# Optimization experiments

Hardware: AMD Instinct MI355X
Metric: run time of the kernel (lower is better)

The kernel has to match this reference:

```python
import jax, jax.numpy as jnp
import numpy as np

S, B, D, H = 2048, 2, 1024, 16
E = D // H  # per-head hidden dim = 64
MASK_VAL = 1e18


def setup_inputs() -> dict:
    rng = jax.random.key(0)
    ks = jax.random.split(rng, 12)
    query = jax.random.normal(ks[0], (S, B, D), dtype=jnp.float32)
    key = jax.random.normal(ks[1], (S, B, D), dtype=jnp.float32)
    value = jax.random.normal(ks[2], (S, B, D), dtype=jnp.float32)
    key_mask = jax.random.randint(ks[3], (S, B), 0, 2).astype(bool)
    # per-head Linear weights stacked: torch Linear is y = x @ W.T + b, W: [out, in]
    Wq = jax.random.normal(ks[4], (H, E, D), dtype=jnp.float32) * 0.02
    bq = jax.random.normal(ks[5], (H, E), dtype=jnp.float32) * 0.02
    Wk = jax.random.normal(ks[6], (H, E, D), dtype=jnp.float32) * 0.02
    bk = jax.random.normal(ks[7], (H, E), dtype=jnp.float32) * 0.02
    Wv = jax.random.normal(ks[8], (H, E, D), dtype=jnp.float32) * 0.02
    bv = jax.random.normal(ks[9], (H, E), dtype=jnp.float32) * 0.02
    Wo = jax.random.normal(ks[10], (D, D), dtype=jnp.float32) * 0.02
    bo = jax.random.normal(ks[11], (D,), dtype=jnp.float32) * 0.02
    return {"query": query, "key": key, "value": value, "key_mask": key_mask,
            "Wq": Wq, "bq": bq, "Wk": Wk, "bk": bk, "Wv": Wv, "bv": bv,
            "Wo": Wo, "bo": bo}


def reference(query, key, value, key_mask, Wq, bq, Wk, bk, Wv, bv, Wo, bo):
    # per-head projections, batched over heads: [S, B, H, E]
    q = jnp.einsum('imd,hed->imhe', query, Wq) + bq
    k = jnp.einsum('imd,hed->imhe', key, Wk) + bk
    v = jnp.einsum('imd,hed->imhe', value, Wv) + bv
    # scores: [H, S_q, B, S_k], scaled by sqrt(per-head dim)
    scores = jnp.einsum('imhe,jmhe->himj', q, k) / jnp.sqrt(jnp.float32(E))
    # key padding mask: key_mask [j, m] -> transpose to [m, j], broadcast over h, i
    scores = scores - key_mask.astype(jnp.float32).T * MASK_VAL
    # causal (forward) mask: strict upper triangle [i, j]
    fwd_mask = jnp.triu(jnp.ones((S, S), dtype=jnp.float32), k=1) * MASK_VAL
    scores = scores - fwd_mask[None, :, None, :]
    attn = jax.nn.softmax(scores, axis=-1)
    # weighted sum: [S, B, H, E]; reshape concatenates heads in order (h outer)
    out = jnp.einsum('himj,jmhe->imhe', attn, v).reshape(S, B, H * E)
    return out @ Wo.T + bo
```

## Files before the change

kernel.cpp:

```cpp
#include <hip/hip_runtime.h>
#include <cmath>

namespace {

constexpr int S = 2048, B = 2, D = 1024, H = 16, E = 64;
constexpr int RM = S * B;
constexpr int K = D;
constexpr int KVB = 64;
constexpr int SEGS_PER_HM = 48;

constexpr float QSCL = 0.18033688011112043f;
constexpr float KMB2 = 1.4426950408889634e18f;

using s16x8 = __attribute__((ext_vector_type(8))) short;
using u16x8 = __attribute__((ext_vector_type(8))) unsigned short;
using f32x4 = __attribute__((ext_vector_type(4))) float;
using u32x2 = __attribute__((ext_vector_type(2))) unsigned;
typedef unsigned short ushort;
typedef unsigned int u32;

__constant__ unsigned char SEG_ORDER[48] = {
    17,0,1,16,44,46,47,15,40,42,43,45,14,36,38,39,41,13,32,34,35,37,
    12,28,30,31,33,11,24,26,27,29,10,20,22,23,25,9,18,19,21,8,7,6,5,4,3,2};

__device__ inline f32x4 mfma16(s16x8 a, s16x8 b, f32x4 c) {
    return __builtin_amdgcn_mfma_f32_16x16x32_bf16(a, b, c, 0, 0, 0);
}

__device__ inline ushort f2bf(float f) {
    unsigned u = __builtin_bit_cast(unsigned, f);
    u += 0x7fffu + ((u >> 16) & 1u);
    return (ushort)(u >> 16);
}

__device__ inline u32 cvtpk_bf16(float lo, float hi) {
    u32 r;
    asm("v_cvt_pk_bf16_f32 %0, %1, %2" : "=v"(r) : "v"(lo), "v"(hi));
    return r;
}

__device__ inline float fexp2(float x) {
#if __has_builtin(__builtin_amdgcn_exp2f)
    return __builtin_amdgcn_exp2f(x);
#else
    return exp2f(x);
#endif
}

__device__ inline void gload_lds16(const void* g, void* l) {
    __builtin_amdgcn_global_load_lds(
        (const __attribute__((address_space(1))) u32*)g,
        (__attribute__((address_space(3))) u32*)l,
        16, 0, 0);
}

__global__ __launch_bounds__(256)
void cvt3_kernel(const float* __restrict__ a, const float* __restrict__ b,
                 const float* __restrict__ c,
                 ushort* __restrict__ ao, ushort* __restrict__ bo2, ushort* __restrict__ co)
{
    const float* src = (blockIdx.y == 0) ? a : (blockIdx.y == 1) ? b : c;
    ushort* dst      = (blockIdx.y == 0) ? ao : (blockIdx.y == 1) ? bo2 : co;
    const size_t i = ((size_t)blockIdx.x * 256 + threadIdx.x) * 8;
    float4 x = *reinterpret_cast<const float4*>(&src[i]);
    float4 y = *reinterpret_cast<const float4*>(&src[i + 4]);
    u16x8 o;
    o[0]=f2bf(x.x); o[1]=f2bf(x.y); o[2]=f2bf(x.z); o[3]=f2bf(x.w);
    o[4]=f2bf(y.x); o[5]=f2bf(y.y); o[6]=f2bf(y.z); o[7]=f2bf(y.w);
    *reinterpret_cast<u16x8*>(&dst[i]) = o;
}

__global__ __launch_bounds__(256)
void cvt4_kernel(const float* __restrict__ a, const float* __restrict__ b,
                 const float* __restrict__ c, const float* __restrict__ d,
                 ushort* __restrict__ ao, ushort* __restrict__ bo2,
                 ushort* __restrict__ co, ushort* __restrict__ dd)
{
    const float* src = (blockIdx.y == 0) ? a : (blockIdx.y == 1) ? b : (blockIdx.y == 2) ? c : d;
    ushort* dst      = (blockIdx.y == 0) ? ao : (blockIdx.y == 1) ? bo2 : (blockIdx.y == 2) ? co : dd;
    const size_t i = ((size_t)blockIdx.x * 256 + threadIdx.x) * 8;
    float4 x = *reinterpret_cast<const float4*>(&src[i]);
    float4 y = *reinterpret_cast<const float4*>(&src[i + 4]);
    u16x8 o;
    o[0]=f2bf(x.x); o[1]=f2bf(x.y); o[2]=f2bf(x.z); o[3]=f2bf(x.w);
    o[4]=f2bf(y.x); o[5]=f2bf(y.y); o[6]=f2bf(y.z); o[7]=f2bf(y.w);
    *reinterpret_cast<u16x8*>(&dst[i]) = o;
}

__device__ inline void mm_core2(const ushort* __restrict__ A, const ushort* __restrict__ W,
                                ushort* Albuf, ushort* Blbuf, int r0, int n0,
                                f32x4 (&acc)[4][2])
{
    const int t  = threadIdx.x;
    const int w  = t >> 6, l = t & 63;
    const int lr = l & 15, lg = l >> 4;
    const int wr = w >> 2, wc = w & 3;
    const int srow = t >> 3;
    const int gch  = (t & 7) ^ (srow & 7);

    auto STAGE = [&](int buf, int kt) {
        #pragma unroll
        for (int c = 0; c < 2; ++c) {
            gload_lds16(&A[(size_t)(r0 + c * 64 + srow) * K + kt + gch * 8],
                        (char*)Albuf + buf * 16384 + c * 8192 + t * 16);
            gload_lds16(&W[(size_t)(n0 + c * 64 + srow) * K + kt + gch * 8],
                        (char*)Blbuf + buf * 16384 + c * 8192 + t * 16);
        }
    };

    STAGE(0, 0);
    __syncthreads();
    int cur = 0;

    for (int kt = 0; kt < K; kt += 64) {
        if (kt + 64 < K) STAGE(cur ^ 1, kt + 64);
        const char* Ab = (const char*)Albuf + cur * 16384;
        const char* Bb = (const char*)Blbuf + cur * 16384;

        #pragma unroll
        for (int ks = 0; ks < 2; ++ks) {
            s16x8 af[4], bf[2];
            #pragma unroll
            for (int mf = 0; mf < 4; ++mf) {
                const int row = wr * 64 + mf * 16 + lr;
                const int ch  = (ks * 4 + lg) ^ (row & 7);
                af[mf] = *reinterpret_cast<const s16x8*>(Ab + row * 128 + ch * 16);
            }
            #pragma unroll
            for (int nf = 0; nf < 2; ++nf) {
                const int row = wc * 32 + nf * 16 + lr;
                const int ch  = (ks * 4 + lg) ^ (row & 7);
                bf[nf] = *reinterpret_cast<const s16x8*>(Bb + row * 128 + ch * 16);
            }
            #pragma unroll
            for (int mf = 0; mf < 4; ++mf)
                #pragma unroll
                for (int nf = 0; nf < 2; ++nf)
                    acc[mf][nf] = mfma16(af[mf], bf[nf], acc[mf][nf]);
        }
        __syncthreads();
        cur ^= 1;
    }
}

__global__ __launch_bounds__(512)
void proj_gemm(const ushort* __restrict__ qa, const ushort* __restrict__ ka,
               const ushort* __restrict__ va,
               const ushort* __restrict__ wq, const ushort* __restrict__ wk,
               const ushort* __restrict__ wv,
               const float* __restrict__ bq, const float* __restrict__ bk,
               const float* __restrict__ bv,
               ushort* __restrict__ qd, ushort* __restrict__ kd, ushort* __restrict__ vtd)
{
    __shared__ ushort Albuf[2 * 128 * 64];
    __shared__ ushort Blbuf[2 * 128 * 64];
    const int z = blockIdx.z;
    const ushort* A    = (z == 0) ? qa : (z == 1) ? ka : va;
    const ushort* W    = (z == 0) ? wq : (z == 1) ? wk : wv;
    const float*  bias = (z == 0) ? bq : (z == 1) ? bk : bv;
    const int r0 = blockIdx.x * 128, n0 = blockIdx.y * 128;

    f32x4 acc[4][2] = {};
    mm_core2(A, W, Albuf, Blbuf, r0, n0, acc);

    const int t = threadIdx.x, w = t >> 6, l = t & 63, lr = l & 15, lg = l >> 4;
    const int wr = w >> 2, wc = w & 3;
    #pragma unroll
    for (int mf = 0; mf < 4; ++mf) {
        #pragma unroll
        for (int nf = 0; nf < 2; ++nf) {
            const int n = n0 + wc * 32 + nf * 16 + lr;
            const int h = n >> 6, e = n & 63;
            const float bb = bias[n];
            #pragma unroll
            for (int rg = 0; rg < 4; ++rg) {
                const int r = r0 + wr * 64 + mf * 16 + lg * 4 + rg;
                const int i = r >> 1, m = r & 1;
                const ushort val = f2bf(acc[mf][nf][rg] + bb);
                if (z < 2) {
                    ushort* dst = (z == 0) ? qd : kd;
                    dst[(((size_t)(h * B + m)) * S + i) * E + e] = val;
                } else {
                    vtd[(((size_t)(h * B + m)) * E + e) * S + i] = val;
                }
            }
        }
    }
}

__global__ __launch_bounds__(512)
void out_gemm(const ushort* __restrict__ A, const ushort* __restrict__ W,
              const float* __restrict__ bias, float* __restrict__ Cout)
{
    __shared__ ushort Albuf[2 * 128 * 64];
    __shared__ ushort Blbuf[2 * 128 * 64];
    const int r0 = blockIdx.x * 128, n0 = blockIdx.y * 128;

    f32x4 acc[4][2] = {};
    mm_core2(A, W, Albuf, Blbuf, r0, n0, acc);

    const int t = threadIdx.x, w = t >> 6, l = t & 63, lr = l & 15, lg = l >> 4;
    const int wr = w >> 2, wc = w & 3;
    #pragma unroll
    for (int mf = 0; mf < 4; ++mf) {
        #pragma unroll
        for (int nf = 0; nf < 2; ++nf) {
            const int n = n0 + wc * 32 + nf * 16 + lr;
            const float bb = bias[n];
            #pragma unroll
            for (int rg = 0; rg < 4; ++rg) {
                const int r = r0 + wr * 64 + mf * 16 + lg * 4 + rg;
                Cout[(size_t)r * D + n] = acc[mf][nf][rg] + bb;
            }
        }
    }
}

__global__ __launch_bounds__(256)
void prescan_kernel(const int* __restrict__ km, int* __restrict__ fu,
                    float* __restrict__ kmf)
{
    __shared__ int red[256];
    const int m = blockIdx.x, t = threadIdx.x;
    int best = S;
    for (int j = t; j < S; j += 256) {
        const int v = km[(size_t)j * B + m];
        kmf[(size_t)m * S + j] = v ? KMB2 : 0.0f;
        if (v == 0) best = min(best, j);
    }
    red[t] = best;
    __syncthreads();
    for (int s = 128; s > 0; s >>= 1) {
        if (t < s) red[t] = min(red[t], red[t + s]);
        __syncthreads();
    }
    if (t == 0) fu[m] = red[0];
}

__device__ inline int nseg_of(int t)  { return (t == 0 || t >= 17) ? 2 : 1; }
__device__ inline int segoff_of(int t){ return (t == 0) ? 0 : (t <= 16 ? t + 1 : 2 * t - 16); }

__global__ __launch_bounds__(256)
void attn_seg(const ushort* __restrict__ q, const ushort* __restrict__ k,
              const ushort* __restrict__ vt, const int* __restrict__ fu,
              const float* __restrict__ kmf,
              float* __restrict__ part_O, float* __restrict__ part_ml)
{
    const int s = SEG_ORDER[blockIdx.x];
    const int m = blockIdx.y, h = blockIdx.z;
    int t, kk;
    if (s < 2)       { t = 0;               kk = s; }
    else if (s < 18) { t = s - 1;           kk = 0; }
    else             { t = 17 + ((s - 18) >> 1); kk = (s - 18) & 1; }
    const int i0 = t * 64;
    const int hm = h * B + m;
    const int seg = hm * SEGS_PER_HM + s;

    const int ns = nseg_of(t);
    const int h1 = (t == 0) ? 16 : ((t + 2) >> 1);
    const int jendT = (fu[m] <= i0) ? (t + 1) : 32;
    const int lo = (ns == 2 && kk == 1) ? h1 : 0;
    const int hi = (ns == 2 && kk == 0) ? min(h1, jendT) : jendT;

    const ushort* Qb  = q  + (size_t)hm * S * E;
    const ushort* Kb  = k  + (size_t)hm * S * E;
    const ushort* Vtb = vt + (size_t)hm * E * S;
    const float*  kmfm = kmf + (size_t)m * S;

    __shared__ ushort Ks[2][KVB * 64];
    __shared__ ushort Vts[2][E * 64];
    __shared__ ushort Pw[4][16 * 64];

    const int tid = threadIdx.x;
    const int wv  = tid >> 6;
    const int l   = tid & 63;
    const int lg  = l >> 4;
    const int lcc = l & 15;
    const int a7  = lcc & 7;
    const int gi  = i0 + wv * 16 + lcc;

    const int srow = tid >> 3;
    const int sch  = (tid & 7) ^ (srow & 7);

    s16x8 qf0, qf1;
    {
        const ushort* qp = &Qb[(size_t)gi * E + lg * 8];
        qf0 = *reinterpret_cast<const s16x8*>(qp);
        qf1 = *reinterpret_cast<const s16x8*>(qp + 32);
    }

    float m_run = -INFINITY, l_run = 0.0f;
    f32x4 oacc[4] = {};

    auto STAGE = [&](int buf, int tj) {
        const int j0 = tj * 64;
        gload_lds16(&Kb[(size_t)(j0 + srow) * E + sch * 8],
                    (char*)&Ks[buf][0] + tid * 16);
        gload_lds16(&Kb[(size_t)(j0 + 32 + srow) * E + sch * 8],
                    (char*)&Ks[buf][0] + 4096 + tid * 16);
        gload_lds16(&Vtb[(size_t)srow * S + j0 + sch * 8],
                    (char*)&Vts[buf][0] + tid * 16);
        gload_lds16(&Vtb[(size_t)(32 + srow) * S + j0 + sch * 8],
                    (char*)&Vts[buf][0] + 4096 + tid * 16);
    };

    STAGE(0, lo);
    __syncthreads();
    int cur = 0;

    for (int tj = lo; tj < hi; ++tj) {
        const int j0 = tj * 64;
        if (tj + 1 < hi) STAGE(cur ^ 1, tj + 1);

        float4 km4[4];
        #pragma unroll
        for (int jt = 0; jt < 4; ++jt)
            km4[jt] = *reinterpret_cast<const float4*>(&kmfm[j0 + jt * 16 + lg * 4]);

        f32x4 sacc[4];
        #pragma unroll
        for (int jt = 0; jt < 4; ++jt) {
            const char* kb = (const char*)&Ks[cur][0] + (jt * 16 + lcc) * 128;
            s16x8 kf0 = *reinterpret_cast<const s16x8*>(kb + (lg ^ a7) * 16);
            s16x8 kf1 = *reinterpret_cast<const s16x8*>(kb + ((lg ^ a7) ^ 4) * 16);
            f32x4 a = {};
            a = mfma16(kf0, qf0, a);
            a = mfma16(kf1, qf1, a);
            sacc[jt] = a;
        }

        if (j0 >= i0) {
            #pragma unroll
            for (int jt = 0; jt < 4; ++jt) {
                const int jmi = j0 + jt * 16 + lg * 4 - gi;
                #pragma unroll
                for (int r = 0; r < 4; ++r) {
                    float sc = fmaf(sacc[jt][r], QSCL, -((const float*)&km4[jt])[r]);
                    sc -= (jmi + r > 0) ? KMB2 : 0.0f;
                    sacc[jt][r] = sc;
                }
            }
        } else {
            #pragma unroll
            for (int jt = 0; jt < 4; ++jt)
                #pragma unroll
                for (int r = 0; r < 4; ++r)
                    sacc[jt][r] = fmaf(sacc[jt][r], QSCL, -((const float*)&km4[jt])[r]);
        }

        float mm = -INFINITY;
        #pragma unroll
        for (int jt = 0; jt < 4; ++jt)
            #pragma unroll
            for (int r = 0; r < 4; ++r) mm = fmaxf(mm, sacc[jt][r]);
        mm = fmaxf(mm, __shfl_xor(mm, 16));
        mm = fmaxf(mm, __shfl_xor(mm, 32));

        if (!__all(mm <= m_run)) {
            const float m_new = fmaxf(m_run, mm);
            const float scale = fexp2(m_run - m_new);
            m_run = m_new;
            l_run *= scale;
            float scr[4];
            #pragma unroll
            for (int r = 0; r < 4; ++r)
                scr[r] = __shfl(scale, (l & 48) | (lg * 4 + r));
            #pragma unroll
            for (int et = 0; et < 4; ++et)
                #pragma unroll
                for (int r = 0; r < 4; ++r) oacc[et][r] *= scr[r];
        }

        float psum = 0.0f;
        #pragma unroll
        for (int jt = 0; jt < 4; ++jt) {
            const float p0 = fexp2(sacc[jt][0] - m_run);
            const float p1 = fexp2(sacc[jt][1] - m_run);
            const float p2 = fexp2(sacc[jt][2] - m_run);
            const float p3 = fexp2(sacc[jt][3] - m_run);
            psum += (p0 + p1) + (p2 + p3);
            const u32 w0 = cvtpk_bf16(p0, p1);
            const u32 w1 = cvtpk_bf16(p2, p3);
            const int pby = lcc * 128 + (((jt * 2 + (lg >> 1)) ^ a7) << 4) + ((lg & 1) << 3);
            *reinterpret_cast<u32x2*>((char*)&Pw[wv][0] + pby) = (u32x2){w0, w1};
        }
        psum += __shfl_xor(psum, 16);
        psum += __shfl_xor(psum, 32);
        l_run += psum;

        {
            const char* pb = (const char*)&Pw[wv][0] + lcc * 128;
            s16x8 pf0 = *reinterpret_cast<const s16x8*>(pb + (lg ^ a7) * 16);
            s16x8 pf1 = *reinterpret_cast<const s16x8*>(pb + ((lg ^ a7) ^ 4) * 16);
            #pragma unroll
            for (int et = 0; et < 4; ++et) {
                const char* vb = (const char*)&Vts[cur][0] + (et * 16 + lcc) * 128;
                s16x8 vf0 = *reinterpret_cast<const s16x8*>(vb + (lg ^ a7) * 16);
                s16x8 vf1 = *reinterpret_cast<const s16x8*>(vb + ((lg ^ a7) ^ 4) * 16);
                oacc[et] = mfma16(pf0, vf0, oacc[et]);
                oacc[et] = mfma16(pf1, vf1, oacc[et]);
            }
        }

        __syncthreads();
        cur ^= 1;
    }

    #pragma unroll
    for (int et = 0; et < 4; ++et)
        #pragma unroll
        for (int r = 0; r < 4; ++r)
            part_O[((size_t)seg * 64 + wv * 16 + lg * 4 + r) * 64 + et * 16 + lcc] = oacc[et][r];
    if (lg == 0) {
        part_ml[((size_t)seg * 64 + wv * 16 + lcc) * 2]     = m_run;
        part_ml[((size_t)seg * 64 + wv * 16 + lcc) * 2 + 1] = l_run;
    }
}

__global__ __launch_bounds__(256)
void attn_combine(const float* __restrict__ part_O, const float* __restrict__ part_ml,
                  ushort* __restrict__ a_ws)
{
    const int t = blockIdx.x, m = blockIdx.y, h = blockIdx.z;
    const int hm = h * B + m;
    const int ns = nseg_of(t);
    const int seg0 = hm * SEGS_PER_HM + segoff_of(t);

    const int tid = threadIdx.x;
    const int row = tid >> 2;
    const int e0  = (tid & 3) * 16;
    const int gi  = t * 64 + row;

    const size_t r0 = (size_t)seg0 * 64 + row;
    const float m0 = part_ml[r0 * 2], l0 = part_ml[r0 * 2 + 1];
    float w0, w1 = 0.0f, linv;
    size_t r1 = 0;
    if (ns == 2) {
        r1 = ((size_t)(seg0 + 1)) * 64 + row;
        const float m1 = part_ml[r1 * 2], l1 = part_ml[r1 * 2 + 1];
        const float ms = fmaxf(m0, m1);
        w0 = fexp2(m0 - ms);
        w1 = fexp2(m1 - ms);
        linv = 1.0f / (l0 * w0 + l1 * w1);
    } else {
        w0 = 1.0f;
        linv = 1.0f / l0;
    }

    ushort* dst = a_ws + ((size_t)gi * B + m) * D + h * E + e0;
    #pragma unroll
    for (int c = 0; c < 4; ++c) {
        float4 o0 = *reinterpret_cast<const float4*>(&part_O[r0 * 64 + e0 + c * 4]);
        float ov[4] = {o0.x, o0.y, o0.z, o0.w};
        if (ns == 2) {
            float4 o1 = *reinterpret_cast<const float4*>(&part_O[r1 * 64 + e0 + c * 4]);
            ov[0] = ov[0] * w0 + o1.x * w1;
            ov[1] = ov[1] * w0 + o1.y * w1;
            ov[2] = ov[2] * w0 + o1.z * w1;
            ov[3] = ov[3] * w0 + o1.w * w1;
        } else {
            ov[0] *= w0; ov[1] *= w0; ov[2] *= w0; ov[3] *= w0;
        }
        dst[c * 4 + 0] = f2bf(ov[0] * linv);
        dst[c * 4 + 1] = f2bf(ov[1] * linv);
        dst[c * 4 + 2] = f2bf(ov[2] * linv);
        dst[c * 4 + 3] = f2bf(ov[3] * linv);
    }
}

}

extern "C" void kernel_launch(void* const* d_in, const int* in_sizes, int n_in,
                              void* d_out, int out_size, void* d_ws, size_t ws_size,
                              hipStream_t stream)
{
    const float* query = (const float*)d_in[0];
    const float* key   = (const float*)d_in[1];
    const float* value = (const float*)d_in[2];
    const int*   kmask = (const int*)  d_in[3];
    const float* Wq    = (const float*)d_in[4];
    const float* bq    = (const float*)d_in[5];
    const float* Wk    = (const float*)d_in[6];
    const float* bk    = (const float*)d_in[7];
    const float* Wv    = (const float*)d_in[8];
    const float* bv    = (const float*)d_in[9];
    const float* Wo    = (const float*)d_in[10];
    const float* bo    = (const float*)d_in[11];
    float* out = (float*)d_out;

    const size_t act = (size_t)RM * D;
    const size_t wsz = (size_t)D * D;
    ushort* wob  = (ushort*)d_ws;
    ushort* wqb  = wob + wsz;
    ushort* wkb  = wqb + wsz;
    ushort* wvb  = wkb + wsz;
    ushort* qa   = wvb + wsz;
    ushort* ka   = qa + act;
    ushort* va   = ka + act;
    ushort* q_ws = va + act;
    ushort* k_ws = q_ws + act;
    ushort* vt_ws= k_ws + act;
    ushort* a_ws = vt_ws + act;
    float* part_O  = (float*)qa;
    float* part_ml = (float*)wqb;
    int*   fu      = (int*)wkb;
    float* kmf     = (float*)wkb + 8;

    cvt3_kernel<<<dim3(act / 8 / 256, 3), 256, 0, stream>>>(query, key, value, qa, ka, va);
    cvt4_kernel<<<dim3(wsz / 8 / 256, 4), 256, 0, stream>>>(Wq, Wk, Wv, Wo, wqb, wkb, wvb, wob);

    proj_gemm<<<dim3(RM / 128, D / 128, 3), 512, 0, stream>>>(
        qa, ka, va, wqb, wkb, wvb, bq, bk, bv, q_ws, k_ws, vt_ws);

    prescan_kernel<<<dim3(B), 256, 0, stream>>>(kmask, fu, kmf);

    attn_seg<<<dim3(SEGS_PER_HM, B, H), 256, 0, stream>>>(
        q_ws, k_ws, vt_ws, fu, kmf, part_O, part_ml);

    attn_combine<<<dim3(S / 64, B, H), 256, 0, stream>>>(part_O, part_ml, a_ws);

    out_gemm<<<dim3(RM / 128, D / 128), 512, 0, stream>>>(a_ws, wob, bo, out);
}
```

Baseline: 148.4 us.

## Remap block indices for XCD-aware L2 locality and raise MFMA wave priority

All three kernels (projection GEMM, output GEMM, attention segments) now remap the linear block index so that consecutive logical tiles land on the same XCD. MI355X dispatches blocks round-robin across 8 XCDs, so the `(lin & 7) * N + (lin >> 3)` remap is meant to let tiles that share inputs reuse the same L2. The attention kernel also wraps its QK and PV MFMA sections in s_setprio so that waves issuing matrix instructions get scheduling priority over waves doing softmax. The remap changes the dispatch order of the attention segments, which could disturb the existing SEG_ORDER load balancing.

```diff
diff --git a/kernel.cpp b/kernel.cpp
--- a/kernel.cpp
+++ b/kernel.cpp
@@ -154,11 +154,15 @@
 {
     __shared__ ushort Albuf[2 * 128 * 64];
     __shared__ ushort Blbuf[2 * 128 * 64];
-    const int z = blockIdx.z;
+    const int lin = blockIdx.x + 32 * (blockIdx.y + 8 * blockIdx.z);
+    const int nf  = (lin & 7) * 96 + (lin >> 3);
+    const int bx  = nf & 31;
+    const int by  = (nf >> 5) & 7;
+    const int z   = nf >> 8;
     const ushort* A    = (z == 0) ? qa : (z == 1) ? ka : va;
     const ushort* W    = (z == 0) ? wq : (z == 1) ? wk : wv;
     const float*  bias = (z == 0) ? bq : (z == 1) ? bk : bv;
-    const int r0 = blockIdx.x * 128, n0 = blockIdx.y * 128;
+    const int r0 = bx * 128, n0 = by * 128;
 
     f32x4 acc[4][2] = {};
     mm_core2(A, W, Albuf, Blbuf, r0, n0, acc);
@@ -168,15 +172,15 @@
     #pragma unroll
     for (int mf = 0; mf < 4; ++mf) {
         #pragma unroll
-        for (int nf = 0; nf < 2; ++nf) {
-            const int n = n0 + wc * 32 + nf * 16 + lr;
+        for (int nf2 = 0; nf2 < 2; ++nf2) {
+            const int n = n0 + wc * 32 + nf2 * 16 + lr;
             const int h = n >> 6, e = n & 63;
             const float bb = bias[n];
             #pragma unroll
             for (int rg = 0; rg < 4; ++rg) {
                 const int r = r0 + wr * 64 + mf * 16 + lg * 4 + rg;
                 const int i = r >> 1, m = r & 1;
-                const ushort val = f2bf(acc[mf][nf][rg] + bb);
+                const ushort val = f2bf(acc[mf][nf2][rg] + bb);
                 if (z < 2) {
                     ushort* dst = (z == 0) ? qd : kd;
                     dst[(((size_t)(h * B + m)) * S + i) * E + e] = val;
@@ -194,7 +198,9 @@
 {
     __shared__ ushort Albuf[2 * 128 * 64];
     __shared__ ushort Blbuf[2 * 128 * 64];
-    const int r0 = blockIdx.x * 128, n0 = blockIdx.y * 128;
+    const int lin = blockIdx.x + 32 * blockIdx.y;
+    const int nf  = (lin & 7) * 32 + (lin >> 3);
+    const int r0 = (nf & 31) * 128, n0 = (nf >> 5) * 128;
 
     f32x4 acc[4][2] = {};
     mm_core2(A, W, Albuf, Blbuf, r0, n0, acc);
@@ -204,13 +210,13 @@
     #pragma unroll
     for (int mf = 0; mf < 4; ++mf) {
         #pragma unroll
-        for (int nf = 0; nf < 2; ++nf) {
-            const int n = n0 + wc * 32 + nf * 16 + lr;
+        for (int nf2 = 0; nf2 < 2; ++nf2) {
+            const int n = n0 + wc * 32 + nf2 * 16 + lr;
             const float bb = bias[n];
             #pragma unroll
             for (int rg = 0; rg < 4; ++rg) {
                 const int r = r0 + wr * 64 + mf * 16 + lg * 4 + rg;
-                Cout[(size_t)r * D + n] = acc[mf][nf][rg] + bb;
+                Cout[(size_t)r * D + n] = acc[mf][nf2][rg] + bb;
             }
         }
     }
@@ -246,8 +252,11 @@
               const float* __restrict__ kmf,
               float* __restrict__ part_O, float* __restrict__ part_ml)
 {
-    const int s = SEG_ORDER[blockIdx.x];
-    const int m = blockIdx.y, h = blockIdx.z;
+    const int lin = blockIdx.x + SEGS_PER_HM * (blockIdx.y + B * blockIdx.z);
+    const int nf  = (lin & 7) * 192 + (lin >> 3);
+    const int s   = SEG_ORDER[nf % SEGS_PER_HM];
+    const int m   = (nf / SEGS_PER_HM) % B;
+    const int h   = nf / (SEGS_PER_HM * B);
     int t, kk;
     if (s < 2)       { t = 0;               kk = s; }
     else if (s < 18) { t = s - 1;           kk = 0; }
@@ -318,6 +327,7 @@
             km4[jt] = *reinterpret_cast<const float4*>(&kmfm[j0 + jt * 16 + lg * 4]);
 
         f32x4 sacc[4];
+        __builtin_amdgcn_s_setprio(1);
         #pragma unroll
         for (int jt = 0; jt < 4; ++jt) {
             const char* kb = (const char*)&Ks[cur][0] + (jt * 16 + lcc) * 128;
@@ -328,6 +338,7 @@
             a = mfma16(kf1, qf1, a);
             sacc[jt] = a;
         }
+        __builtin_amdgcn_s_setprio(0);
 
         if (j0 >= i0) {
             #pragma unroll
@@ -390,6 +401,7 @@
 
         {
             const char* pb = (const char*)&Pw[wv][0] + lcc * 128;
+            __builtin_amdgcn_s_setprio(1);
             s16x8 pf0 = *reinterpret_cast<const s16x8*>(pb + (lg ^ a7) * 16);
             s16x8 pf1 = *reinterpret_cast<const s16x8*>(pb + ((lg ^ a7) ^ 4) * 16);
             #pragma unroll
@@ -400,6 +412,7 @@
                 oacc[et] = mfma16(pf0, vf0, oacc[et]);
                 oacc[et] = mfma16(pf1, vf1, oacc[et]);
             }
+            __builtin_amdgcn_s_setprio(0);
         }
 
         __syncthreads();
```

Result: slower. 154.4 us, median of 2 (+4.1%).
